# Kernel tuning notes

Measured on AMD Instinct MI355X. Metric: run time of the kernel, lower is better.

## Reference

```python
import jax, jax.numpy as jnp
import numpy as np

# static config (matches init_kwargs and a standard 4-level FPN for ~800px input)
SPATIAL_SHAPES = ((100, 100), (50, 50), (25, 25), (13, 13))  # (H_l, W_l)
B, C, H, L, P = 2, 256, 8, 4, 4
DFFN = 2048
DH = C // H
LQ = sum(h * w for h, w in SPATIAL_SHAPES)  # 13294


def layer_norm(x, g, b, eps=1e-5):
    m = jnp.mean(x, -1, keepdims=True)
    v = jnp.mean((x - m) ** 2, -1, keepdims=True)
    return (x - m) * jax.lax.rsqrt(v + eps) * g + b


def ms_deform_sample(value, loc, attn):
    # value [B,Lv,H,DH], loc [B,Lq,H,L,P,2] in [0,1], attn [B,Lq,H,L,P]
    value = jnp.transpose(value, (0, 2, 1, 3))  # [B,H,Lv,DH]
    lq = loc.shape[1]
    out = jnp.zeros((B, H, lq, DH), value.dtype)
    start = 0
    for l, (Hl, Wl) in enumerate(SPATIAL_SHAPES):
        v = jax.lax.dynamic_slice_in_dim(value, start, Hl * Wl, axis=2)  # [B,H,N_l,DH]
        # grid_sample(align_corners=False) coords: x = loc_x*W - 0.5
        gx = jnp.transpose(loc[:, :, :, l, :, 0], (0, 2, 1, 3)) * Wl - 0.5  # [B,H,Lq,P]
        gy = jnp.transpose(loc[:, :, :, l, :, 1], (0, 2, 1, 3)) * Hl - 0.5
        aw = jnp.transpose(attn[:, :, :, l, :], (0, 2, 1, 3))  # [B,H,Lq,P]
        x0 = jnp.floor(gx)
        y0 = jnp.floor(gy)
        for dx in (0.0, 1.0):
            for dy in (0.0, 1.0):
                xi = x0 + dx
                yi = y0 + dy
                w = (1.0 - jnp.abs(gx - xi)) * (1.0 - jnp.abs(gy - yi))
                valid = (xi >= 0) & (xi < Wl) & (yi >= 0) & (yi < Hl)
                idx = (jnp.clip(yi, 0, Hl - 1) * Wl + jnp.clip(xi, 0, Wl - 1)).astype(jnp.int32)
                g = jnp.take_along_axis(v, idx.reshape(B, H, -1)[..., None], axis=2)  # [B,H,Lq*P,DH]
                ww = (w * aw * valid.astype(w.dtype))[..., None]  # [B,H,Lq,P,1]
                out = out + jnp.sum(g.reshape(B, H, lq, P, DH) * ww, axis=3)
        start += Hl * Wl
    return jnp.transpose(out, (0, 2, 1, 3)).reshape(B, lq, C)


def setup_inputs() -> dict:
    key = jax.random.key(0)
    ks = jax.random.split(key, 16)
    s = 0.02
    return {
        "src": jax.random.normal(ks[0], (B, LQ, C), jnp.float32),
        "pos": jax.random.normal(ks[1], (B, LQ, C), jnp.float32),
        "reference_points": jax.random.uniform(ks[2], (B, LQ, L, 2), jnp.float32),
        "w_value": jax.random.normal(ks[3], (C, C), jnp.float32) * s,
        "b_value": jnp.zeros((C,), jnp.float32),
        "w_off": jax.random.normal(ks[4], (C, H * L * P * 2), jnp.float32) * s,
        "b_off": jax.random.normal(ks[5], (H * L * P * 2,), jnp.float32) * s,
        "w_attn": jax.random.normal(ks[6], (C, H * L * P), jnp.float32) * s,
        "b_attn": jnp.zeros((H * L * P,), jnp.float32),
        "w_out": jax.random.normal(ks[7], (C, C), jnp.float32) * s,
        "b_out": jnp.zeros((C,), jnp.float32),
        "ln1_g": jnp.ones((C,), jnp.float32),
        "ln1_b": jnp.zeros((C,), jnp.float32),
        "w_ffn1": jax.random.normal(ks[8], (C, DFFN), jnp.float32) * s,
        "b_ffn1": jnp.zeros((DFFN,), jnp.float32),
        "w_ffn2": jax.random.normal(ks[9], (DFFN, C), jnp.float32) * s,
        "b_ffn2": jnp.zeros((C,), jnp.float32),
        "ln2_g": jnp.ones((C,), jnp.float32),
        "ln2_b": jnp.zeros((C,), jnp.float32),
    }


def reference(src, pos, reference_points, w_value, b_value, w_off, b_off, w_attn, b_attn,
              w_out, b_out, ln1_g, ln1_b, w_ffn1, b_ffn1, w_ffn2, b_ffn2, ln2_g, ln2_b):
    # DeformableTransformerEncoderLayer.forward (eval mode, no dropout)
    q = src + pos  # with_pos_embed
    lq = q.shape[1]
    value = (src @ w_value + b_value).reshape(B, -1, H, DH)
    off = (q @ w_off + b_off).reshape(B, lq, H, L, P, 2)
    attn = (q @ w_attn + b_attn).reshape(B, lq, H, L * P)
    attn = jax.nn.softmax(attn, axis=-1).reshape(B, lq, H, L, P)
    # offset_normalizer = (W_l, H_l)
    norm = jnp.array([[w, h] for h, w in SPATIAL_SHAPES], dtype=src.dtype)
    loc = reference_points[:, :, None, :, None, :] + off / norm[None, None, None, :, None, :]
    src2 = ms_deform_sample(value, loc, attn) @ w_out + b_out
    x = layer_norm(src + src2, ln1_g, ln1_b)
    ff = jax.nn.relu(x @ w_ffn1 + b_ffn1) @ w_ffn2 + b_ffn2
    return layer_norm(x + ff, ln2_g, ln2_b)
```

## Files before the change

### kernel.cpp

```cpp
#include <hip/hip_runtime.h>

#define LQN   13294
#define NBAT  2
#define MROWS (NBAT * LQN)
#define CCH   256
#define NHEAD 8
#define DHEAD 32
#define NLVL  4
#define NPT   4
#define DFF   2048

typedef short short8 __attribute__((ext_vector_type(8)));
typedef float f32x4 __attribute__((ext_vector_type(4)));
typedef unsigned short u16;
typedef u16 u16x4 __attribute__((ext_vector_type(4)));

__device__ __forceinline__ u16 f2bf(float f) {
  unsigned int u = __builtin_bit_cast(unsigned int, f);
  u += 0x7fffu + ((u >> 16) & 1u);
  return (u16)(u >> 16);
}
__device__ __forceinline__ float bf2f(u16 s) {
  unsigned int u = ((unsigned int)s) << 16;
  return __builtin_bit_cast(float, u);
}
__device__ __forceinline__ void async16(const void* g, void* l) {
  __builtin_amdgcn_global_load_lds(
      (const __attribute__((address_space(1))) void*)g,
      (__attribute__((address_space(3))) void*)l, 16, 0, 0);
}

template<int OUT_MODE>
__global__ __launch_bounds__(256, 2)
void gemm_bf16(const u16* __restrict__ A, const u16* __restrict__ BT,
               const float* __restrict__ bias, void* __restrict__ Cout,
               int M, int N, int K)
{
  __shared__ u16 As[2][128 * 64];
  __shared__ u16 Bs[2][128 * 64];
  const int t    = threadIdx.x;
  const int lane = t & 63;
  const int wid  = t >> 6;
  const int wm   = wid >> 1, wn = wid & 1;
  const int bm   = blockIdx.x, bn = blockIdx.y;
  const int l15  = lane & 15;
  const int kq   = lane >> 4;

  f32x4 acc[4][4];
#pragma unroll
  for (int m = 0; m < 4; ++m)
#pragma unroll
    for (int n = 0; n < 4; ++n) acc[m][n] = (f32x4)0.0f;

  auto stage = [&](int buf, int kt) {
#pragma unroll
    for (int i = 0; i < 4; ++i) {
      const int c   = i * 256 + t;
      const int row = c >> 3;
      const int kg  = (c & 7) ^ (row & 7);
      int ar = bm * 128 + row; ar = ar < M ? ar : M - 1;
      async16(&A[(size_t)ar * K + kt + kg * 8], &As[buf][c * 8]);
      const int br = bn * 128 + row;
      async16(&BT[(size_t)br * K + kt + kg * 8], &Bs[buf][c * 8]);
    }
  };

  stage(0, 0);
  __syncthreads();
  int cur = 0;

  for (int kt = 0; kt < K; kt += 64) {
    if (kt + 64 < K) stage(cur ^ 1, kt + 64);

#pragma unroll
    for (int kk = 0; kk < 2; ++kk) {
      short8 af[4], bfr[4];
#pragma unroll
      for (int m = 0; m < 4; ++m) {
        const int row = wm * 64 + m * 16 + l15;
        const int xb  = (kk * 64 + kq * 16) ^ ((row & 7) << 4);
        af[m] = *(const short8*)((const char*)&As[cur][0] + row * 128 + xb);
      }
#pragma unroll
      for (int n = 0; n < 4; ++n) {
        const int col = wn * 64 + n * 16 + l15;
        const int xb  = (kk * 64 + kq * 16) ^ ((col & 7) << 4);
        bfr[n] = *(const short8*)((const char*)&Bs[cur][0] + col * 128 + xb);
      }
#pragma unroll
      for (int m = 0; m < 4; ++m)
#pragma unroll
        for (int n = 0; n < 4; ++n)
          acc[m][n] = __builtin_amdgcn_mfma_f32_16x16x32_bf16(af[m], bfr[n], acc[m][n], 0, 0, 0);
    }

    __syncthreads();
    cur ^= 1;
  }

  const int crow0 = bm * 128 + wm * 64;
  const int ccol0 = bn * 128 + wn * 64;
#pragma unroll
  for (int n = 0; n < 4; ++n) {
    int col = ccol0 + n * 16 + l15;
    float bv = bias[col];
#pragma unroll
    for (int m = 0; m < 4; ++m) {
      int rbase = crow0 + m * 16 + kq * 4;
#pragma unroll
      for (int j = 0; j < 4; ++j) {
        int row = rbase + j;
        if (row < M) {
          float v = acc[m][n][j] + bv;
          if constexpr (OUT_MODE == 0) ((float*)Cout)[(size_t)row * N + col] = v;
          else                         ((u16*)Cout)[(size_t)row * N + col] = f2bf(v);
        }
      }
    }
  }
}

__global__ __launch_bounds__(256, 2)
void gemm_dual(const u16* __restrict__ A0, const u16* __restrict__ BT0,
               const float* __restrict__ bias0, u16* __restrict__ C0,
               const u16* __restrict__ A1, const u16* __restrict__ BT1,
               const float* __restrict__ bias1, float* __restrict__ C1)
{
  __shared__ u16 As[2][128 * 64];
  __shared__ u16 Bs[2][128 * 64];
  const int t    = threadIdx.x;
  const int lane = t & 63;
  const int wid  = t >> 6;
  const int wm   = wid >> 1, wn = wid & 1;
  const int bm   = blockIdx.x;
  const int bnG  = blockIdx.y;
  const bool first = bnG < 2;
  const u16* A    = first ? A0 : A1;
  const u16* BT   = first ? BT0 : BT1;
  const float* bias = first ? bias0 : bias1;
  const int  N    = first ? 256 : 384;
  const int  bn   = first ? bnG : bnG - 2;
  const int l15  = lane & 15;
  const int kq   = lane >> 4;

  f32x4 acc[4][4];
#pragma unroll
  for (int m = 0; m < 4; ++m)
#pragma unroll
    for (int n = 0; n < 4; ++n) acc[m][n] = (f32x4)0.0f;

  auto stage = [&](int buf, int kt) {
#pragma unroll
    for (int i = 0; i < 4; ++i) {
      const int c   = i * 256 + t;
      const int row = c >> 3;
      const int kg  = (c & 7) ^ (row & 7);
      int ar = bm * 128 + row; ar = ar < MROWS ? ar : MROWS - 1;
      async16(&A[(size_t)ar * 256 + kt + kg * 8], &As[buf][c * 8]);
      const int br = bn * 128 + row;
      async16(&BT[(size_t)br * 256 + kt + kg * 8], &Bs[buf][c * 8]);
    }
  };

  stage(0, 0);
  __syncthreads();
  int cur = 0;

  for (int kt = 0; kt < 256; kt += 64) {
    if (kt + 64 < 256) stage(cur ^ 1, kt + 64);

#pragma unroll
    for (int kk = 0; kk < 2; ++kk) {
      short8 af[4], bfr[4];
#pragma unroll
      for (int m = 0; m < 4; ++m) {
        const int row = wm * 64 + m * 16 + l15;
        const int xb  = (kk * 64 + kq * 16) ^ ((row & 7) << 4);
        af[m] = *(const short8*)((const char*)&As[cur][0] + row * 128 + xb);
      }
#pragma unroll
      for (int n = 0; n < 4; ++n) {
        const int col = wn * 64 + n * 16 + l15;
        const int xb  = (kk * 64 + kq * 16) ^ ((col & 7) << 4);
        bfr[n] = *(const short8*)((const char*)&Bs[cur][0] + col * 128 + xb);
      }
#pragma unroll
      for (int m = 0; m < 4; ++m)
#pragma unroll
        for (int n = 0; n < 4; ++n)
          acc[m][n] = __builtin_amdgcn_mfma_f32_16x16x32_bf16(af[m], bfr[n], acc[m][n], 0, 0, 0);
    }

    __syncthreads();
    cur ^= 1;
  }

  const int crow0 = bm * 128 + wm * 64;
  const int ccol0 = bn * 128 + wn * 64;
#pragma unroll
  for (int n = 0; n < 4; ++n) {
    int col = ccol0 + n * 16 + l15;
    float bv = bias[col];
#pragma unroll
    for (int m = 0; m < 4; ++m) {
      int rbase = crow0 + m * 16 + kq * 4;
#pragma unroll
      for (int j = 0; j < 4; ++j) {
        int row = rbase + j;
        if (row < MROWS) {
          float v = acc[m][n][j] + bv;
          if (first) C0[(size_t)row * 256 + col] = f2bf(v);
          else       C1[(size_t)row * 384 + col] = v;
        }
      }
    }
  }
}

__global__ __launch_bounds__(512, 2)
void ffn_fused(const u16* __restrict__ x_bf, const u16* __restrict__ W1T,
               const u16* __restrict__ W2T, const float* __restrict__ b1,
               const float* __restrict__ b2, float* __restrict__ out)
{
  extern __shared__ char smem[];
  u16* w1s = (u16*)(smem);
  u16* w2s = (u16*)(smem + 65536);
  char* ps = (char*)(smem + 131072);

  const int t    = threadIdx.x;
  const int lane = t & 63;
  const int wid  = t >> 6;
  const int l15  = lane & 15;
  const int kq   = lane >> 4;
  const int bm   = blockIdx.x;
  const int pwm  = wid >> 1, pwn = wid & 1;
  const int wm   = wid >> 2, wn = wid & 3;

  short8 xr[2][8];
#pragma unroll
  for (int m = 0; m < 2; ++m) {
    int ar = bm * 128 + pwm * 32 + m * 16 + l15;
    ar = ar < MROWS ? ar : MROWS - 1;
    const char* xb = (const char*)x_bf + (size_t)ar * 512 + kq * 16;
#pragma unroll
    for (int ks = 0; ks < 8; ++ks)
      xr[m][ks] = *(const short8*)(xb + ks * 64);
  }

  auto stage = [&](int buf, int it) {
#pragma unroll
    for (int i = 0; i < 4; ++i) {
      const int c  = i * 512 + t;
      const int r1 = c >> 5;
      const int k1 = ((c & 31) ^ (r1 & 7)) * 8;
      async16(&W1T[(size_t)(it * 64 + r1) * 256 + k1], &w1s[buf * 16384 + c * 8]);
      const int r2 = c >> 3;
      const int k2 = ((c & 7) ^ (r2 & 7)) * 8;
      async16(&W2T[(size_t)r2 * 2048 + it * 64 + k2], &w2s[buf * 16384 + c * 8]);
    }
  };

  f32x4 acc[4][4];
#pragma unroll
  for (int m = 0; m < 4; ++m)
#pragma unroll
    for (int n = 0; n < 4; ++n) acc[m][n] = (f32x4)0.0f;

  stage(0, 0);
  __syncthreads();

  for (int it = 0; it < 32; ++it) {
    const int cur = it & 1;
    if (it < 31) stage(cur ^ 1, it + 1);

    f32x4 p[2][2];
#pragma unroll
    for (int m = 0; m < 2; ++m)
#pragma unroll
      for (int n = 0; n < 2; ++n) p[m][n] = (f32x4)0.0f;

#pragma unroll
    for (int ks = 0; ks < 8; ++ks) {
      short8 bfr[2];
#pragma unroll
      for (int n = 0; n < 2; ++n) {
        const int wrow = pwn * 32 + n * 16 + l15;
        const int xb   = (ks * 64 + kq * 16) ^ ((wrow & 7) << 4);
        bfr[n] = *(const short8*)((const char*)&w1s[cur * 16384] + wrow * 512 + xb);
      }
#pragma unroll
      for (int m = 0; m < 2; ++m)
#pragma unroll
        for (int n = 0; n < 2; ++n)
          p[m][n] = __builtin_amdgcn_mfma_f32_16x16x32_bf16(xr[m][ks], bfr[n], p[m][n], 0, 0, 0);
    }

#pragma unroll
    for (int n = 0; n < 2; ++n) {
      const int col = pwn * 32 + n * 16 + l15;
      const float bv = b1[it * 64 + col];
      const int chnk = col >> 3;
      const int sub  = (col & 7) * 2;
#pragma unroll
      for (int m = 0; m < 2; ++m)
#pragma unroll
        for (int j = 0; j < 4; ++j) {
          const int prow = pwm * 32 + m * 16 + kq * 4 + j;
          const float v = fmaxf(p[m][n][j] + bv, 0.0f);
          *(u16*)(ps + prow * 160 + ((chnk ^ ((prow >> 2) & 3)) << 4) + sub) = f2bf(v);
        }
    }
    __syncthreads();

#pragma unroll
    for (int kk = 0; kk < 2; ++kk) {
      short8 paf[4], bfr[4];
#pragma unroll
      for (int m = 0; m < 4; ++m) {
        const int arow = wm * 64 + m * 16 + l15;
        const int c    = kk * 4 + kq;
        paf[m] = *(const short8*)(ps + arow * 160 + ((c ^ ((arow >> 2) & 3)) << 4));
      }
#pragma unroll
      for (int n = 0; n < 4; ++n) {
        const int brow = wn * 64 + n * 16 + l15;
        const int xb   = ((kk * 4 + kq) ^ (brow & 7)) * 16;
        bfr[n] = *(const short8*)((const char*)&w2s[cur * 16384] + brow * 128 + xb);
      }
#pragma unroll
      for (int m = 0; m < 4; ++m)
#pragma unroll
        for (int n = 0; n < 4; ++n)
          acc[m][n] = __builtin_amdgcn_mfma_f32_16x16x32_bf16(paf[m], bfr[n], acc[m][n], 0, 0, 0);
    }
    __syncthreads();
  }

  const int crow0 = bm * 128 + wm * 64;
#pragma unroll
  for (int n = 0; n < 4; ++n) {
    const int col = wn * 64 + n * 16 + l15;
    const float bv = b2[col];
#pragma unroll
    for (int m = 0; m < 4; ++m) {
      const int rbase = crow0 + m * 16 + kq * 4;
#pragma unroll
      for (int j = 0; j < 4; ++j) {
        const int row = rbase + j;
        if (row < MROWS) out[(size_t)row * 256 + col] = acc[m][n][j] + bv;
      }
    }
  }
}

__global__ __launch_bounds__(256)
void sampler_kernel(const float* __restrict__ offattn,
                    const float* __restrict__ refp,
                    const u16*  __restrict__ value,
                    u16*        __restrict__ src2)
{
  __shared__ float2 sWI[4][8][65];

  const int t    = threadIdx.x;
  const int r4   = t >> 6;
  const int lane = t & 63;
  const int row  = blockIdx.x * 4 + r4;
  const int b    = row / LQN;

  {
    const float* oa = offattn + (size_t)row * 384;
    const float* rp = refp + (size_t)row * 8;
    const int p16 = lane & 15;
    const int l   = p16 >> 2;
    const int Wl  = (l == 0) ? 100 : (l == 1) ? 50 : (l == 2) ? 25 : 13;
    const int st  = (l == 0) ? 0 : (l == 1) ? 10000 : (l == 2) ? 12500 : 13125;
    const float rx = rp[l * 2 + 0] * (float)Wl - 0.5f;
    const float ry = rp[l * 2 + 1] * (float)Wl - 0.5f;

#pragma unroll
    for (int s = 0; s < 2; ++s) {
      const int h = s * 4 + (lane >> 4);
      float logit = oa[256 + h * 16 + p16];
      float mx = logit;
#pragma unroll
      for (int o = 1; o < 16; o <<= 1) mx = fmaxf(mx, __shfl_xor(mx, o, 64));
      float e = __expf(logit - mx);
      float ssum = e;
#pragma unroll
      for (int o = 1; o < 16; o <<= 1) ssum += __shfl_xor(ssum, o, 64);
      const float aw = e / ssum;

      const float ox = oa[(h * 16 + p16) * 2 + 0];
      const float oy = oa[(h * 16 + p16) * 2 + 1];
      const float gx = rx + ox;
      const float gy = ry + oy;
      const float x0f = floorf(gx), y0f = floorf(gy);
      const int   x0 = (int)x0f, y0 = (int)y0f;
      const float fx = gx - x0f, fy = gy - y0f;
#pragma unroll
      for (int c = 0; c < 4; ++c) {
        const int dx = c & 1, dy = c >> 1;
        const int xi = x0 + dx, yi = y0 + dy;
        const float wx = dx ? fx : 1.0f - fx;
        const float wy = dy ? fy : 1.0f - fy;
        const bool valid = (xi >= 0) && (xi < Wl) && (yi >= 0) && (yi < Wl);
        const int xc = min(max(xi, 0), Wl - 1);
        const int yc = min(max(yi, 0), Wl - 1);
        const int idx = st + yc * Wl + xc;
        const float w = wx * wy * aw * (valid ? 1.0f : 0.0f);
        sWI[r4][h][p16 * 4 + c] = make_float2(w, __builtin_bit_cast(float, idx));
      }
    }
  }
  __syncthreads();

  {
    const int h  = lane >> 3;
    const int c4 = lane & 7;
    const char* vbase = (const char*)value + (size_t)b * LQN * 512 + h * 64 + c4 * 8;
    const float2* wi = sWI[r4][h];

    float a0 = 0.f, a1 = 0.f, a2 = 0.f, a3 = 0.f;
#pragma unroll 16
    for (int e = 0; e < 64; ++e) {
      const float2 p = wi[e];
      const float w  = p.x;
      const int  idx = __builtin_bit_cast(int, p.y);
      const unsigned long long u = *(const unsigned long long*)(vbase + (size_t)idx * 512);
      a0 += w * bf2f((u16)(u));
      a1 += w * bf2f((u16)(u >> 16));
      a2 += w * bf2f((u16)(u >> 32));
      a3 += w * bf2f((u16)(u >> 48));
    }
    u16x4 o;
    o[0] = f2bf(a0); o[1] = f2bf(a1); o[2] = f2bf(a2); o[3] = f2bf(a3);
    *(u16x4*)&src2[(size_t)row * 256 + h * 32 + c4 * 4] = o;
  }
}

template<int WRITE_BF>
__global__ __launch_bounds__(256)
void ln_kernel(const float* __restrict__ Xa, const float* __restrict__ Xb,
               const float* __restrict__ gam, const float* __restrict__ bet,
               float* __restrict__ Yf, u16* __restrict__ Ybf)
{
  const int wid = threadIdx.x >> 6, lane = threadIdx.x & 63;
  const int row = blockIdx.x * 4 + wid;
  const f32x4 va = ((const f32x4*)(Xa + (size_t)row * 256))[lane];
  const f32x4 vb = ((const f32x4*)(Xb + (size_t)row * 256))[lane];
  f32x4 v = va + vb;
  float s1 = v[0] + v[1] + v[2] + v[3];
  float s2 = v[0] * v[0] + v[1] * v[1] + v[2] * v[2] + v[3] * v[3];
#pragma unroll
  for (int off = 32; off; off >>= 1) {
    s1 += __shfl_xor(s1, off, 64);
    s2 += __shfl_xor(s2, off, 64);
  }
  const float mean = s1 * (1.0f / 256.0f);
  const float var  = s2 * (1.0f / 256.0f) - mean * mean;
  const float rstd = rsqrtf(var + 1e-5f);
  const f32x4 gv = ((const f32x4*)gam)[lane];
  const f32x4 bv = ((const f32x4*)bet)[lane];
  f32x4 y;
#pragma unroll
  for (int j = 0; j < 4; ++j) y[j] = (v[j] - mean) * rstd * gv[j] + bv[j];
  ((f32x4*)(Yf + (size_t)row * 256))[lane] = y;
  if constexpr (WRITE_BF) {
    u16x4 o;
#pragma unroll
    for (int j = 0; j < 4; ++j) o[j] = f2bf(y[j]);
    ((u16x4*)(Ybf + (size_t)row * 256))[lane] = o;
  }
}

__global__ __launch_bounds__(256)
void prep_qsrc(const float* __restrict__ src, const float* __restrict__ pos,
               u16* __restrict__ src_bf, u16* __restrict__ q_bf)
{
  const size_t i = (size_t)blockIdx.x * 256 + threadIdx.x;
  const f32x4 s = ((const f32x4*)src)[i];
  const f32x4 p = ((const f32x4*)pos)[i];
  u16x4 sb, qb;
#pragma unroll
  for (int j = 0; j < 4; ++j) { sb[j] = f2bf(s[j]); qb[j] = f2bf(s[j] + p[j]); }
  ((u16x4*)src_bf)[i] = sb;
  ((u16x4*)q_bf)[i]   = qb;
}

__global__ __launch_bounds__(256)
void prep_weights(const float* __restrict__ w_value, const float* __restrict__ w_off,
                  const float* __restrict__ w_attn,  const float* __restrict__ w_out,
                  const float* __restrict__ w_ffn1,  const float* __restrict__ w_ffn2,
                  const float* __restrict__ b_off,   const float* __restrict__ b_attn,
                  u16* __restrict__ WT_val, u16* __restrict__ WT_oa, u16* __restrict__ WT_out,
                  u16* __restrict__ WT_f1,  u16* __restrict__ WT_f2, float* __restrict__ bias_oa)
{
  int i = blockIdx.x * 256 + threadIdx.x;
  if (i < 65536) {
    const int k = i >> 8, n = i & 255;
    WT_val[n * 256 + k] = f2bf(w_value[i]);
  } else if ((i -= 65536) < 65536) {
    const int k = i >> 8, n = i & 255;
    WT_oa[n * 256 + k] = f2bf(w_off[i]);
  } else if ((i -= 65536) < 32768) {
    const int k = i >> 7, n = i & 127;
    WT_oa[(256 + n) * 256 + k] = f2bf(w_attn[i]);
  } else if ((i -= 32768) < 65536) {
    const int k = i >> 8, n = i & 255;
    WT_out[n * 256 + k] = f2bf(w_out[i]);
  } else if ((i -= 65536) < 524288) {
    const int k = i >> 11, n = i & 2047;
    WT_f1[n * 256 + k] = f2bf(w_ffn1[i]);
  } else if ((i -= 524288) < 524288) {
    const int k = i >> 8, n = i & 255;
    WT_f2[n * 2048 + k] = f2bf(w_ffn2[i]);
  } else if ((i -= 524288) < 384) {
    bias_oa[i] = (i < 256) ? b_off[i] : b_attn[i - 256];
  }
}

extern "C" void kernel_launch(void* const* d_in, const int* in_sizes, int n_in,
                              void* d_out, int out_size, void* d_ws, size_t ws_size,
                              hipStream_t stream)
{
  const float* src     = (const float*)d_in[0];
  const float* pos     = (const float*)d_in[1];
  const float* refp    = (const float*)d_in[2];
  const float* w_value = (const float*)d_in[3];
  const float* b_value = (const float*)d_in[4];
  const float* w_off   = (const float*)d_in[5];
  const float* b_off   = (const float*)d_in[6];
  const float* w_attn  = (const float*)d_in[7];
  const float* b_attn  = (const float*)d_in[8];
  const float* w_out   = (const float*)d_in[9];
  const float* b_out   = (const float*)d_in[10];
  const float* ln1_g   = (const float*)d_in[11];
  const float* ln1_b   = (const float*)d_in[12];
  const float* w_ffn1  = (const float*)d_in[13];
  const float* b_ffn1  = (const float*)d_in[14];
  const float* w_ffn2  = (const float*)d_in[15];
  const float* b_ffn2  = (const float*)d_in[16];
  const float* ln2_g   = (const float*)d_in[17];
  const float* ln2_b   = (const float*)d_in[18];

  char* ws = (char*)d_ws;
  size_t off = 0;
  auto alloc = [&](size_t bytes) { void* p = ws + off; off += (bytes + 255) & ~(size_t)255; return p; };

  u16*   src_bf   = (u16*)  alloc((size_t)MROWS * 256 * 2);
  u16*   q_bf     = (u16*)  alloc((size_t)MROWS * 256 * 2);
  float* offattn  = (float*)alloc((size_t)MROWS * 384 * 4);
  u16*   value_bf = (u16*)  alloc((size_t)MROWS * 256 * 2);
  u16*   src2_bf  = (u16*)  alloc((size_t)MROWS * 256 * 2);
  float* x_f32    = (float*)alloc((size_t)MROWS * 256 * 4);
  u16*   WT_val   = (u16*)  alloc(256 * 256 * 2);
  u16*   WT_oa    = (u16*)  alloc(384 * 256 * 2);
  u16*   WT_out   = (u16*)  alloc(256 * 256 * 2);
  u16*   WT_f1    = (u16*)  alloc(2048 * 256 * 2);
  u16*   WT_f2    = (u16*)  alloc((size_t)256 * 2048 * 2);
  float* bias_oa  = (float*)alloc(384 * 4);

  float* src2p = offattn;
  u16*   x_bf  = q_bf;
  float* ff    = (float*)value_bf;

  prep_weights<<<4994, 256, 0, stream>>>(w_value, w_off, w_attn, w_out, w_ffn1, w_ffn2,
                                         b_off, b_attn,
                                         WT_val, WT_oa, WT_out, WT_f1, WT_f2, bias_oa);

  prep_qsrc<<<6647, 256, 0, stream>>>(src, pos, src_bf, q_bf);

  static bool attr_set = false;
  if (!attr_set) {
    hipFuncSetAttribute((const void*)ffn_fused,
                        hipFuncAttributeMaxDynamicSharedMemorySize, 151552);
    attr_set = true;
  }

  gemm_dual<<<dim3(208, 5), 256, 0, stream>>>(src_bf, WT_val, b_value, value_bf,
                                              q_bf, WT_oa, bias_oa, offattn);

  sampler_kernel<<<MROWS / 4, 256, 0, stream>>>(offattn, refp, value_bf, src2_bf);

  gemm_bf16<0><<<dim3(208, 2), 256, 0, stream>>>(src2_bf, WT_out, b_out, src2p, MROWS, 256, 256);

  ln_kernel<1><<<6647, 256, 0, stream>>>(src, src2p, ln1_g, ln1_b, x_f32, x_bf);

  ffn_fused<<<208, 512, 151552, stream>>>(x_bf, WT_f1, WT_f2, b_ffn1, b_ffn2, ff);

  ln_kernel<0><<<6647, 256, 0, stream>>>(x_f32, ff, ln2_g, ln2_b, (float*)d_out, nullptr);
}
```

Baseline: 246.4 us.

## Double ffn_fused block to 1024 threads with smaller per-wave tiles

Reworks the fused FFN kernel to use 16 waves per block instead of 8, giving each wave half the rows in both the FFN1 and FFN2 stages. Weight staging per thread is halved. The intermediate activation buffer drops its XOR swizzle for a padded 144-byte row stride. This aims to raise latency hiding and occupancy within a CU. It risks more barrier cost, lower per-wave register reuse of B fragments, and possible LDS bank conflicts.

```diff
diff --git a/kernel.cpp b/kernel.cpp
--- a/kernel.cpp
+++ b/kernel.cpp
@@ -138,7 +138,6 @@
   const u16* A    = first ? A0 : A1;
   const u16* BT   = first ? BT0 : BT1;
   const float* bias = first ? bias0 : bias1;
-  const int  N    = first ? 256 : 384;
   const int  bn   = first ? bnG : bnG - 2;
   const int l15  = lane & 15;
   const int kq   = lane >> 4;
@@ -217,15 +216,15 @@
   }
 }
 
-__global__ __launch_bounds__(512, 2)
+__global__ __launch_bounds__(1024, 4)
 void ffn_fused(const u16* __restrict__ x_bf, const u16* __restrict__ W1T,
                const u16* __restrict__ W2T, const float* __restrict__ b1,
                const float* __restrict__ b2, float* __restrict__ out)
 {
   extern __shared__ char smem[];
-  u16* w1s = (u16*)(smem);
-  u16* w2s = (u16*)(smem + 65536);
-  char* ps = (char*)(smem + 131072);
+  u16*  w1s = (u16*)(smem);
+  u16*  w2s = (u16*)(smem + 65536);
+  char* ps  = smem + 131072;
 
   const int t    = threadIdx.x;
   const int lane = t & 63;
@@ -234,23 +233,21 @@
   const int kq   = lane >> 4;
   const int bm   = blockIdx.x;
   const int pwm  = wid >> 1, pwn = wid & 1;
-  const int wm   = wid >> 2, wn = wid & 3;
-
-  short8 xr[2][8];
-#pragma unroll
-  for (int m = 0; m < 2; ++m) {
-    int ar = bm * 128 + pwm * 32 + m * 16 + l15;
+  const int vwm  = wid >> 2, vwn = wid & 3;
+
+  short8 xr[8];
+  {
+    int ar = bm * 128 + pwm * 16 + l15;
     ar = ar < MROWS ? ar : MROWS - 1;
     const char* xb = (const char*)x_bf + (size_t)ar * 512 + kq * 16;
 #pragma unroll
-    for (int ks = 0; ks < 8; ++ks)
-      xr[m][ks] = *(const short8*)(xb + ks * 64);
+    for (int ks = 0; ks < 8; ++ks) xr[ks] = *(const short8*)(xb + ks * 64);
   }
 
   auto stage = [&](int buf, int it) {
 #pragma unroll
-    for (int i = 0; i < 4; ++i) {
-      const int c  = i * 512 + t;
+    for (int i = 0; i < 2; ++i) {
+      const int c  = i * 1024 + t;
       const int r1 = c >> 5;
       const int k1 = ((c & 31) ^ (r1 & 7)) * 8;
       async16(&W1T[(size_t)(it * 64 + r1) * 256 + k1], &w1s[buf * 16384 + c * 8]);
@@ -260,9 +257,9 @@
     }
   };
 
-  f32x4 acc[4][4];
-#pragma unroll
-  for (int m = 0; m < 4; ++m)
+  f32x4 acc[2][4];
+#pragma unroll
+  for (int m = 0; m < 2; ++m)
 #pragma unroll
     for (int n = 0; n < 4; ++n) acc[m][n] = (f32x4)0.0f;
 
@@ -273,77 +270,59 @@
     const int cur = it & 1;
     if (it < 31) stage(cur ^ 1, it + 1);
 
-    f32x4 p[2][2];
-#pragma unroll
-    for (int m = 0; m < 2; ++m)
-#pragma unroll
-      for (int n = 0; n < 2; ++n) p[m][n] = (f32x4)0.0f;
-
+    f32x4 p[2];
+    p[0] = (f32x4)0.0f; p[1] = (f32x4)0.0f;
 #pragma unroll
     for (int ks = 0; ks < 8; ++ks) {
-      short8 bfr[2];
 #pragma unroll
       for (int n = 0; n < 2; ++n) {
         const int wrow = pwn * 32 + n * 16 + l15;
-        const int xb   = (ks * 64 + kq * 16) ^ ((wrow & 7) << 4);
-        bfr[n] = *(const short8*)((const char*)&w1s[cur * 16384] + wrow * 512 + xb);
-      }
-#pragma unroll
-      for (int m = 0; m < 2; ++m)
-#pragma unroll
-        for (int n = 0; n < 2; ++n)
-          p[m][n] = __builtin_amdgcn_mfma_f32_16x16x32_bf16(xr[m][ks], bfr[n], p[m][n], 0, 0, 0);
+        const int xb   = (((ks * 4 + kq) ^ (wrow & 7)) << 4);
+        const short8 bfr = *(const short8*)((const char*)&w1s[cur * 16384] + wrow * 512 + xb);
+        p[n] = __builtin_amdgcn_mfma_f32_16x16x32_bf16(xr[ks], bfr, p[n], 0, 0, 0);
+      }
     }
 
 #pragma unroll
     for (int n = 0; n < 2; ++n) {
       const int col = pwn * 32 + n * 16 + l15;
       const float bv = b1[it * 64 + col];
-      const int chnk = col >> 3;
-      const int sub  = (col & 7) * 2;
-#pragma unroll
-      for (int m = 0; m < 2; ++m)
-#pragma unroll
-        for (int j = 0; j < 4; ++j) {
-          const int prow = pwm * 32 + m * 16 + kq * 4 + j;
-          const float v = fmaxf(p[m][n][j] + bv, 0.0f);
-          *(u16*)(ps + prow * 160 + ((chnk ^ ((prow >> 2) & 3)) << 4) + sub) = f2bf(v);
-        }
+#pragma unroll
+      for (int j = 0; j < 4; ++j) {
+        const int prow = pwm * 16 + kq * 4 + j;
+        *(u16*)(ps + prow * 144 + col * 2) = f2bf(fmaxf(p[n][j] + bv, 0.0f));
+      }
     }
     __syncthreads();
 
 #pragma unroll
     for (int kk = 0; kk < 2; ++kk) {
-      short8 paf[4], bfr[4];
-#pragma unroll
-      for (int m = 0; m < 4; ++m) {
-        const int arow = wm * 64 + m * 16 + l15;
-        const int c    = kk * 4 + kq;
-        paf[m] = *(const short8*)(ps + arow * 160 + ((c ^ ((arow >> 2) & 3)) << 4));
+      short8 paf[2];
+#pragma unroll
+      for (int m = 0; m < 2; ++m) {
+        const int arow = vwm * 32 + m * 16 + l15;
+        paf[m] = *(const short8*)(ps + arow * 144 + (kk * 4 + kq) * 16);
       }
 #pragma unroll
       for (int n = 0; n < 4; ++n) {
-        const int brow = wn * 64 + n * 16 + l15;
-        const int xb   = ((kk * 4 + kq) ^ (brow & 7)) * 16;
-        bfr[n] = *(const short8*)((const char*)&w2s[cur * 16384] + brow * 128 + xb);
-      }
-#pragma unroll
-      for (int m = 0; m < 4; ++m)
-#pragma unroll
-        for (int n = 0; n < 4; ++n)
-          acc[m][n] = __builtin_amdgcn_mfma_f32_16x16x32_bf16(paf[m], bfr[n], acc[m][n], 0, 0, 0);
+        const int brow = vwn * 64 + n * 16 + l15;
+        const int xb   = (((kk * 4 + kq) ^ (brow & 7)) << 4);
+        const short8 bfr = *(const short8*)((const char*)&w2s[cur * 16384] + brow * 128 + xb);
+#pragma unroll
+        for (int m = 0; m < 2; ++m)
+          acc[m][n] = __builtin_amdgcn_mfma_f32_16x16x32_bf16(paf[m], bfr, acc[m][n], 0, 0, 0);
+      }
     }
     __syncthreads();
   }
 
-  const int crow0 = bm * 128 + wm * 64;
 #pragma unroll
   for (int n = 0; n < 4; ++n) {
-    const int col = wn * 64 + n * 16 + l15;
+    const int col = vwn * 64 + n * 16 + l15;
     const float bv = b2[col];
 #pragma unroll
-    for (int m = 0; m < 4; ++m) {
-      const int rbase = crow0 + m * 16 + kq * 4;
+    for (int m = 0; m < 2; ++m) {
+      const int rbase = bm * 128 + vwm * 32 + m * 16 + kq * 4;
 #pragma unroll
       for (int j = 0; j < 4; ++j) {
         const int row = rbase + j;
@@ -573,7 +552,7 @@
   static bool attr_set = false;
   if (!attr_set) {
     hipFuncSetAttribute((const void*)ffn_fused,
-                        hipFuncAttributeMaxDynamicSharedMemorySize, 151552);
+                        hipFuncAttributeMaxDynamicSharedMemorySize, 149504);
     attr_set = true;
   }
 
@@ -586,7 +565,7 @@
 
   ln_kernel<1><<<6647, 256, 0, stream>>>(src, src2p, ln1_g, ln1_b, x_f32, x_bf);
 
-  ffn_fused<<<208, 512, 151552, stream>>>(x_bf, WT_f1, WT_f2, b_ffn1, b_ffn2, ff);
+  ffn_fused<<<208, 1024, 149504, stream>>>(x_bf, WT_f1, WT_f2, b_ffn1, b_ffn2, ff);
 
   ln_kernel<0><<<6647, 256, 0, stream>>>(x_f32, ff, ln2_g, ln2_b, (float*)d_out, nullptr);
 }
```

Measured after the change: 252.7 us. +2.5%, slower.
